# Kernel optimization log

Measured on AMD Instinct MI355X. Metric: run time of the kernel, lower is better.

Reference implementation:

```python
import jax, jax.numpy as jnp
import numpy as np

B, T, D, H = 4, 2048, 1024, 16
HD = D // H  # 64


def setup_inputs() -> dict:
    key = jax.random.key(0)
    ks = jax.random.split(key, 5)
    return {
        "x": jax.random.normal(ks[0], (B, T, D), dtype=jnp.float32),
        "W_qkv": jax.random.normal(ks[1], (D, 3 * D), dtype=jnp.float32) * 0.02,
        "b_qkv": jax.random.normal(ks[2], (3 * D,), dtype=jnp.float32) * 0.02,
        "W_out": jax.random.normal(ks[3], (D, D), dtype=jnp.float32) * 0.02,
        "b_out": jax.random.normal(ks[4], (D,), dtype=jnp.float32) * 0.02,
        "mask": 1,
    }


def reference(x, W_qkv, b_qkv, W_out, b_out, mask):
    # fused QKV projection: (B,T,3D)
    qkv = x @ W_qkv + b_qkv
    # torch layout: view (B,T,H,3*hd) then chunk last dim into q,k,v
    qkv = qkv.reshape(B, T, H, 3, HD)
    q = qkv[..., 0, :].transpose(0, 2, 1, 3)  # (B,H,T,hd)
    k = qkv[..., 1, :].transpose(0, 2, 1, 3)
    v = qkv[..., 2, :].transpose(0, 2, 1, 3)
    scores = jnp.einsum('bhqd,bhkd->bhqk', q, k) / jnp.sqrt(jnp.float32(HD))
    if mask:
        causal = jnp.triu(jnp.ones((T, T), dtype=bool), k=1)
        scores = jnp.where(causal[None, None], jnp.float32(-jnp.inf), scores)
    attn = jax.nn.softmax(scores, axis=-1)
    out = jnp.einsum('bhqk,bhkd->bhqd', attn, v)  # (B,H,T,hd)
    out = out.transpose(0, 2, 1, 3).reshape(B, T, D)
    return out @ W_out + b_out
```

## Files before the change

kernel.cpp:

```cpp
#include <hip/hip_runtime.h>

typedef unsigned short u16;
typedef __bf16 bf16x8 __attribute__((ext_vector_type(8)));
typedef float f32x4 __attribute__((ext_vector_type(4)));
typedef float f32x16 __attribute__((ext_vector_type(16)));

#define DEV __device__ __forceinline__

constexpr int Bb = 4, Tt = 2048, Dd = 1024, Hh = 16, HDd = 64;
constexpr int MM = Bb * Tt;
constexpr float QSCALE = 0.125f * 1.4426950408889634f;

DEV u16 f2bf(float f) {
  unsigned u = __float_as_uint(f);
  u += 0x7fffu + ((u >> 16) & 1u);
  return (u16)(u >> 16);
}

DEV unsigned cvtpk(float a, float b) {
  unsigned r;
  asm("v_cvt_pk_bf16_f32 %0, %1, %2" : "=v"(r) : "v"(a), "v"(b));
  return r;
}

DEV void pswap(unsigned& a, unsigned& b) {
  asm("v_permlane32_swap_b32 %0, %1" : "+v"(a), "+v"(b));
}

DEV void gload_lds16(const u16* g, u16* l) {
  __builtin_amdgcn_global_load_lds(
      (const __attribute__((address_space(1))) void*)g,
      (__attribute__((address_space(3))) void*)l, 16, 0, 0);
}

__global__ __launch_bounds__(256) void cast_x_kernel(const float* __restrict__ in,
                                                     u16* __restrict__ out, int n8) {
  int i = blockIdx.x * 256 + threadIdx.x;
  if (i >= n8) return;
  const float4* p = (const float4*)in + (size_t)i * 2;
  float4 v0 = p[0], v1 = p[1];
  union { u16 u[8]; uint4 v; } t;
  t.u[0] = f2bf(v0.x); t.u[1] = f2bf(v0.y); t.u[2] = f2bf(v0.z); t.u[3] = f2bf(v0.w);
  t.u[4] = f2bf(v1.x); t.u[5] = f2bf(v1.y); t.u[6] = f2bf(v1.z); t.u[7] = f2bf(v1.w);
  ((uint4*)out)[i] = t.v;
}

__global__ __launch_bounds__(256) void wcast_t_kernel(const float* __restrict__ in,
                                                      u16* __restrict__ out, int K, int N) {
  __shared__ float tile[32][33];
  int n0 = blockIdx.x * 32, k0 = blockIdx.y * 32;
  int tx = threadIdx.x & 31, ty = threadIdx.x >> 5;
  #pragma unroll
  for (int yy = ty; yy < 32; yy += 8)
    tile[yy][tx] = in[(size_t)(k0 + yy) * N + n0 + tx];
  __syncthreads();
  #pragma unroll
  for (int yy = ty; yy < 32; yy += 8)
    out[(size_t)(n0 + yy) * K + k0 + tx] = f2bf(tile[tx][yy]);
}

__global__ __launch_bounds__(256) void vtrans_kernel(const u16* __restrict__ V,
                                                     u16* __restrict__ Vt) {
  __shared__ u16 tile[32][33];
  size_t base = (size_t)blockIdx.z * Tt * HDd;
  int t0 = blockIdx.x * 32, d0 = blockIdx.y * 32;
  int tx = threadIdx.x & 31, ty = threadIdx.x >> 5;
  #pragma unroll
  for (int yy = ty; yy < 32; yy += 8)
    tile[yy][tx] = V[base + (size_t)(t0 + yy) * HDd + d0 + tx];
  __syncthreads();
  #pragma unroll
  for (int yy = ty; yy < 32; yy += 8)
    Vt[base + (size_t)(d0 + yy) * Tt + t0 + tx] = tile[tx][yy];
}

DEV void stage_tile(const u16* __restrict__ src, int row0, int k0, int ld, u16* lds) {
  int t = threadIdx.x, w = t >> 6;
  #pragma unroll
  for (int j = 0; j < 2; ++j) {
    int e = (j * 256 + t) * 8;
    int r = e >> 5;
    int slot = (e >> 3) & 3;
    int c = (slot ^ ((r >> 1) & 3)) << 3;
    gload_lds16(src + (size_t)(row0 + r) * ld + k0 + c, lds + j * 2048 + w * 512);
  }
}

template <int EPI>
__global__ __launch_bounds__(256) void gemm_bt_kernel(
    const u16* __restrict__ A, const u16* __restrict__ Bt,
    const float* __restrict__ bias, float* __restrict__ Cf,
    u16* __restrict__ Qb, u16* __restrict__ Kb, u16* __restrict__ Vb,
    int M, int N, int Kd) {
  __shared__ __align__(16) u16 As[2][4096];
  __shared__ __align__(16) u16 Bs[2][4096];
  int m0 = blockIdx.y * 128, n0 = blockIdx.x * 128;
  int tid = threadIdx.x, l = tid & 63, w = tid >> 6;
  int lo = l & 15, g = l >> 4;
  int wm = (w >> 1) * 64, wn = (w & 1) * 64;
  f32x4 acc[4][4] = {};
  stage_tile(A, m0, 0, Kd, As[0]);
  stage_tile(Bt, n0, 0, Kd, Bs[0]);
  __syncthreads();
  int nk = Kd >> 5;
  for (int kt = 0; kt < nk; ++kt) {
    int cur = kt & 1;
    if (kt + 1 < nk) {
      stage_tile(A, m0, (kt + 1) * 32, Kd, As[cur ^ 1]);
      stage_tile(Bt, n0, (kt + 1) * 32, Kd, Bs[cur ^ 1]);
    }
    bf16x8 a[4], b[4];
    #pragma unroll
    for (int i = 0; i < 4; ++i) {
      int row = wm + i * 16 + lo;
      a[i] = *(const bf16x8*)&As[cur][row * 32 + ((g ^ ((row >> 1) & 3)) << 3)];
    }
    #pragma unroll
    for (int j = 0; j < 4; ++j) {
      int row = wn + j * 16 + lo;
      b[j] = *(const bf16x8*)&Bs[cur][row * 32 + ((g ^ ((row >> 1) & 3)) << 3)];
    }
    #pragma unroll
    for (int i = 0; i < 4; ++i)
      #pragma unroll
      for (int j = 0; j < 4; ++j)
        acc[i][j] = __builtin_amdgcn_mfma_f32_16x16x32_bf16(a[i], b[j], acc[i][j], 0, 0, 0);
    __syncthreads();
  }
  #pragma unroll
  for (int j = 0; j < 4; ++j) {
    int n = n0 + wn + j * 16 + lo;
    float bv = bias[n];
    #pragma unroll
    for (int i = 0; i < 4; ++i) {
      #pragma unroll
      for (int r = 0; r < 4; ++r) {
        int m = m0 + wm + i * 16 + g * 4 + r;
        float v = acc[i][j][r] + bv;
        if (EPI == 0) {
          int b_ = m >> 11, t = m & (Tt - 1);
          int h = n / 192, sub = n - h * 192;
          int which = sub >> 6, d = sub & 63;
          size_t idx = ((size_t)(b_ * Hh + h) * Tt + t) * HDd + d;
          if (which == 0)      Qb[idx] = f2bf(v * QSCALE);
          else if (which == 1) Kb[idx] = f2bf(v);
          else                 Vb[idx] = f2bf(v);
        } else {
          Cf[(size_t)m * N + n] = v;
        }
      }
    }
  }
}

DEV void stage64x64(const u16* __restrict__ g, size_t rstride, u16* lds) {
  int t = threadIdx.x, w = t >> 6;
  #pragma unroll
  for (int j = 0; j < 2; ++j) {
    int e = j * 256 + t;
    int r = e >> 3, p = e & 7;
    int lg = p ^ (r & 7);
    gload_lds16(g + (size_t)r * rstride + lg * 8, lds + (size_t)(j * 256 + w * 64) * 8);
  }
}

DEV void build_pfrags(const f32x16& s, bf16x8& f0, bf16x8& f1) {
  unsigned w0 = cvtpk(s[0], s[1]),  w1 = cvtpk(s[2], s[3]);
  unsigned w2 = cvtpk(s[4], s[5]),  w3 = cvtpk(s[6], s[7]);
  unsigned w4 = cvtpk(s[8], s[9]),  w5 = cvtpk(s[10], s[11]);
  unsigned w6 = cvtpk(s[12], s[13]), w7 = cvtpk(s[14], s[15]);
  pswap(w0, w2);
  pswap(w1, w3);
  pswap(w4, w6);
  pswap(w5, w7);
  union { unsigned u[4]; bf16x8 v; } t0, t1;
  t0.u[0] = w0; t0.u[1] = w1; t0.u[2] = w2; t0.u[3] = w3;
  t1.u[0] = w4; t1.u[1] = w5; t1.u[2] = w6; t1.u[3] = w7;
  f0 = t0.v; f1 = t1.v;
}

DEV void write_o(u16* __restrict__ O, size_t rowbase, const f32x16& o0,
                 const f32x16& o1, float L, int hf) {
  float inv = 1.0f / L;
  #pragma unroll
  for (int m = 0; m < 4; ++m) {
    uint2 v0, v1;
    v0.x = cvtpk(o0[4 * m] * inv,     o0[4 * m + 1] * inv);
    v0.y = cvtpk(o0[4 * m + 2] * inv, o0[4 * m + 3] * inv);
    *(uint2*)(O + rowbase + m * 8 + hf * 4) = v0;
    v1.x = cvtpk(o1[4 * m] * inv,     o1[4 * m + 1] * inv);
    v1.y = cvtpk(o1[4 * m + 2] * inv, o1[4 * m + 3] * inv);
    *(uint2*)(O + rowbase + 32 + m * 8 + hf * 4) = v1;
  }
}

__global__ __launch_bounds__(256) void attn_kernel(const u16* __restrict__ Q,
                                                   const u16* __restrict__ K,
                                                   const u16* __restrict__ Vt,
                                                   u16* __restrict__ O) {
  __shared__ __align__(16) u16 Ks[2][4096];
  __shared__ __align__(16) u16 Vs[2][4096];
  int bh = blockIdx.y;
  int b_ = bh >> 4, h = bh & 15;
  const u16* Qp = Q + (size_t)bh * Tt * HDd;
  const u16* Kp = K + (size_t)bh * Tt * HDd;
  const u16* Vp = Vt + (size_t)bh * HDd * Tt;
  int tid = threadIdx.x, w = tid >> 6, l = tid & 63;
  int lq = l & 31, hf = l >> 5;
  int p = blockIdx.x;
  int JA = 15 - p, JB = p;
  int ntA = 2 * JA + 2, ntB = 2 * JB + 2, ntT = ntA + ntB;

  int q0 = 128 * JA + 32 * w;
  int qrow = q0 + lq;

  bf16x8 aq[4];
  #pragma unroll
  for (int s = 0; s < 4; ++s)
    aq[s] = *(const bf16x8*)(Qp + (size_t)qrow * HDd + s * 16 + hf * 8);

  f32x16 o0 = {}, o1 = {};
  float M = -1e30f, L = 0.f;

  stage64x64(Kp, HDd, Ks[0]);
  stage64x64(Vp, Tt, Vs[0]);
  __syncthreads();

  for (int it = 0; it < ntT; ++it) {
    if (it == ntA) {
      size_t rbA = ((size_t)b_ * Tt + qrow) * Dd + h * HDd;
      write_o(O, rbA, o0, o1, L, hf);
      #pragma unroll
      for (int r = 0; r < 16; ++r) { o0[r] = 0.f; o1[r] = 0.f; }
      M = -1e30f; L = 0.f;
      q0 = 128 * JB + 32 * w;
      qrow = q0 + lq;
      #pragma unroll
      for (int s = 0; s < 4; ++s)
        aq[s] = *(const bf16x8*)(Qp + (size_t)qrow * HDd + s * 16 + hf * 8);
    }
    int kt = (it < ntA ? it : it - ntA) * 64;
    int cur = it & 1;
    if (it + 1 < ntT) {
      int nkt = (it + 1 < ntA ? it + 1 : it + 1 - ntA) * 64;
      stage64x64(Kp + (size_t)nkt * HDd, HDd, Ks[cur ^ 1]);
      stage64x64(Vp + nkt, Tt, Vs[cur ^ 1]);
    }
    if (kt < q0 + 32) {
      f32x16 s0 = {}, s1 = {};
      int swz = lq & 7;
      __builtin_amdgcn_s_setprio(1);
      #pragma unroll
      for (int ds = 0; ds < 4; ++ds) {
        int slot = 2 * ds + hf;
        bf16x8 k0 = *(const bf16x8*)&Ks[cur][lq * 64 + ((slot ^ swz) << 3)];
        bf16x8 k1 = *(const bf16x8*)&Ks[cur][(32 + lq) * 64 + ((slot ^ swz) << 3)];
        s0 = __builtin_amdgcn_mfma_f32_32x32x16_bf16(k0, aq[ds], s0, 0, 0, 0);
        s1 = __builtin_amdgcn_mfma_f32_32x32x16_bf16(k1, aq[ds], s1, 0, 0, 0);
      }
      __builtin_amdgcn_s_setprio(0);
      if (kt + 63 > q0) {
        #pragma unroll
        for (int r = 0; r < 16; ++r) {
          int kg = kt + (r & 3) + 8 * (r >> 2) + 4 * hf;
          if (kg > qrow)      s0[r] = -INFINITY;
          if (kg + 32 > qrow) s1[r] = -INFINITY;
        }
      }
      float mx_[16];
      #pragma unroll
      for (int r = 0; r < 16; ++r) mx_[r] = fmaxf(s0[r], s1[r]);
      #pragma unroll
      for (int st = 8; st >= 1; st >>= 1)
        #pragma unroll
        for (int r = 0; r < 16; ++r) if (r < st) mx_[r] = fmaxf(mx_[r], mx_[r + st]);
      float mx = fmaxf(mx_[0], __shfl_xor(mx_[0], 32));
      float Mn = fmaxf(M, mx);
      float sc = __builtin_amdgcn_exp2f(M - Mn);
      M = Mn;
      #pragma unroll
      for (int r = 0; r < 16; ++r) {
        s0[r] = __builtin_amdgcn_exp2f(s0[r] - Mn);
        s1[r] = __builtin_amdgcn_exp2f(s1[r] - Mn);
      }
      float ls_[16];
      #pragma unroll
      for (int r = 0; r < 16; ++r) ls_[r] = s0[r] + s1[r];
      #pragma unroll
      for (int st = 8; st >= 1; st >>= 1)
        #pragma unroll
        for (int r = 0; r < 16; ++r) if (r < st) ls_[r] += ls_[r + st];
      float ls = ls_[0] + __shfl_xor(ls_[0], 32);
      L = L * sc + ls;
      bf16x8 pf0, pf1, pf2, pf3;
      build_pfrags(s0, pf0, pf1);
      build_pfrags(s1, pf2, pf3);
      #pragma unroll
      for (int r = 0; r < 16; ++r) { o0[r] *= sc; o1[r] *= sc; }
      __builtin_amdgcn_s_setprio(1);
      #pragma unroll
      for (int ks = 0; ks < 4; ++ks) {
        int slot = 2 * ks + hf;
        bf16x8 v0 = *(const bf16x8*)&Vs[cur][lq * 64 + ((slot ^ swz) << 3)];
        bf16x8 v1 = *(const bf16x8*)&Vs[cur][(32 + lq) * 64 + ((slot ^ swz) << 3)];
        bf16x8 pf = (ks == 0) ? pf0 : (ks == 1) ? pf1 : (ks == 2) ? pf2 : pf3;
        o0 = __builtin_amdgcn_mfma_f32_32x32x16_bf16(v0, pf, o0, 0, 0, 0);
        o1 = __builtin_amdgcn_mfma_f32_32x32x16_bf16(v1, pf, o1, 0, 0, 0);
      }
      __builtin_amdgcn_s_setprio(0);
    }
    __syncthreads();
  }

  size_t rbB = ((size_t)b_ * Tt + qrow) * Dd + h * HDd;
  write_o(O, rbB, o0, o1, L, hf);
}

extern "C" void kernel_launch(void* const* d_in, const int* in_sizes, int n_in,
                              void* d_out, int out_size, void* d_ws, size_t ws_size,
                              hipStream_t stream) {
  const float* x    = (const float*)d_in[0];
  const float* Wqkv = (const float*)d_in[1];
  const float* bqkv = (const float*)d_in[2];
  const float* Wout = (const float*)d_in[3];
  const float* bout = (const float*)d_in[4];
  float* out = (float*)d_out;
  char* ws = (char*)d_ws;

  u16* xb    = (u16*)(ws + 0);
  u16* Wqkvt = (u16*)(ws + 16777216);
  u16* Woutt = (u16*)(ws + 23068672);
  u16* Qb    = (u16*)(ws + 25165824);
  u16* Kb    = (u16*)(ws + 41943040);
  u16* Vb    = (u16*)(ws + 58720256);
  u16* Vtb   = (u16*)(ws + 0);
  u16* Ob    = (u16*)(ws + 58720256);

  cast_x_kernel<<<4096, 256, 0, stream>>>(x, xb, (MM * Dd) / 8);
  wcast_t_kernel<<<dim3(96, 32), 256, 0, stream>>>(Wqkv, Wqkvt, Dd, 3 * Dd);
  wcast_t_kernel<<<dim3(32, 32), 256, 0, stream>>>(Wout, Woutt, Dd, Dd);
  gemm_bt_kernel<0><<<dim3(24, 64), 256, 0, stream>>>(
      xb, Wqkvt, bqkv, nullptr, Qb, Kb, Vb, MM, 3 * Dd, Dd);
  vtrans_kernel<<<dim3(Tt / 32, HDd / 32, Bb * Hh), 256, 0, stream>>>(Vb, Vtb);
  attn_kernel<<<dim3(8, Bb * Hh), 256, 0, stream>>>(Qb, Kb, Vtb, Ob);
  gemm_bt_kernel<1><<<dim3(8, 64), 256, 0, stream>>>(
      Ob, Woutt, bout, out, nullptr, nullptr, nullptr, MM, Dd, Dd);
}
```

Measured before the change: 205.1 us.

## Stage QKV epilogue through LDS, swizzle GEMM tile order, skip lazy softmax rescale

The QKV GEMM epilogue now writes bf16 results into a swizzled LDS buffer per wave, then stores coalesced 16-byte rows to the head-major Q/K/V layout. Previously each lane did scattered 2-byte stores. Workgroup IDs are remapped so that neighbouring blocks share A/B tiles for better L2 reuse. The flash-attention loop skips the running-max update and output rescale unless the new max exceeds the old one by more than 8 (log2 units), trading a small overflow-headroom risk for fewer rescales.

```diff
diff --git a/kernel.cpp b/kernel.cpp
--- a/kernel.cpp
+++ b/kernel.cpp
@@ -92,33 +92,39 @@
     const float* __restrict__ bias, float* __restrict__ Cf,
     u16* __restrict__ Qb, u16* __restrict__ Kb, u16* __restrict__ Vb,
     int M, int N, int Kd) {
-  __shared__ __align__(16) u16 As[2][4096];
-  __shared__ __align__(16) u16 Bs[2][4096];
-  int m0 = blockIdx.y * 128, n0 = blockIdx.x * 128;
+  __shared__ __align__(16) u16 SH[16384];
+  int nx = N >> 7;
+  int bid = blockIdx.y * nx + blockIdx.x;
+  int nwg = (M >> 7) * nx;
+  int swz = (bid & 7) * (nwg >> 3) + (bid >> 3);
+  int m0 = (swz / nx) * 128, n0 = (swz % nx) * 128;
+
   int tid = threadIdx.x, l = tid & 63, w = tid >> 6;
   int lo = l & 15, g = l >> 4;
   int wm = (w >> 1) * 64, wn = (w & 1) * 64;
   f32x4 acc[4][4] = {};
-  stage_tile(A, m0, 0, Kd, As[0]);
-  stage_tile(Bt, n0, 0, Kd, Bs[0]);
+  stage_tile(A, m0, 0, Kd, SH);
+  stage_tile(Bt, n0, 0, Kd, SH + 8192);
   __syncthreads();
   int nk = Kd >> 5;
   for (int kt = 0; kt < nk; ++kt) {
     int cur = kt & 1;
     if (kt + 1 < nk) {
-      stage_tile(A, m0, (kt + 1) * 32, Kd, As[cur ^ 1]);
-      stage_tile(Bt, n0, (kt + 1) * 32, Kd, Bs[cur ^ 1]);
-    }
+      stage_tile(A, m0, (kt + 1) * 32, Kd, SH + (cur ^ 1) * 4096);
+      stage_tile(Bt, n0, (kt + 1) * 32, Kd, SH + 8192 + (cur ^ 1) * 4096);
+    }
+    const u16* Ac = SH + cur * 4096;
+    const u16* Bc = SH + 8192 + cur * 4096;
     bf16x8 a[4], b[4];
     #pragma unroll
     for (int i = 0; i < 4; ++i) {
       int row = wm + i * 16 + lo;
-      a[i] = *(const bf16x8*)&As[cur][row * 32 + ((g ^ ((row >> 1) & 3)) << 3)];
+      a[i] = *(const bf16x8*)&Ac[row * 32 + ((g ^ ((row >> 1) & 3)) << 3)];
     }
     #pragma unroll
     for (int j = 0; j < 4; ++j) {
       int row = wn + j * 16 + lo;
-      b[j] = *(const bf16x8*)&Bs[cur][row * 32 + ((g ^ ((row >> 1) & 3)) << 3)];
+      b[j] = *(const bf16x8*)&Bc[row * 32 + ((g ^ ((row >> 1) & 3)) << 3)];
     }
     #pragma unroll
     for (int i = 0; i < 4; ++i)
@@ -127,26 +133,48 @@
         acc[i][j] = __builtin_amdgcn_mfma_f32_16x16x32_bf16(a[i], b[j], acc[i][j], 0, 0, 0);
     __syncthreads();
   }
-  #pragma unroll
-  for (int j = 0; j < 4; ++j) {
-    int n = n0 + wn + j * 16 + lo;
-    float bv = bias[n];
-    #pragma unroll
-    for (int i = 0; i < 4; ++i) {
-      #pragma unroll
-      for (int r = 0; r < 4; ++r) {
-        int m = m0 + wm + i * 16 + g * 4 + r;
-        float v = acc[i][j][r] + bv;
-        if (EPI == 0) {
-          int b_ = m >> 11, t = m & (Tt - 1);
-          int h = n / 192, sub = n - h * 192;
-          int which = sub >> 6, d = sub & 63;
-          size_t idx = ((size_t)(b_ * Hh + h) * Tt + t) * HDd + d;
-          if (which == 0)      Qb[idx] = f2bf(v * QSCALE);
-          else if (which == 1) Kb[idx] = f2bf(v);
-          else                 Vb[idx] = f2bf(v);
-        } else {
-          Cf[(size_t)m * N + n] = v;
+  if (EPI == 0) {
+    u16* ep = SH + w * 4096;
+    int nblk = n0 + wn;
+    int hh = nblk / 192, which = (nblk % 192) >> 6;
+    float qs = (which == 0) ? QSCALE : 1.0f;
+    #pragma unroll
+    for (int j = 0; j < 4; ++j) {
+      float bv = bias[nblk + j * 16 + lo];
+      int slot = j * 2 + (lo >> 3);
+      #pragma unroll
+      for (int i = 0; i < 4; ++i) {
+        #pragma unroll
+        for (int r = 0; r < 4; ++r) {
+          int lrow = i * 16 + g * 4 + r;
+          ep[lrow * 64 + ((slot ^ (lrow & 7)) << 3) + (lo & 7)] =
+              f2bf((acc[i][j][r] + bv) * qs);
+        }
+      }
+    }
+    asm volatile("s_waitcnt lgkmcnt(0)" ::: "memory");
+    u16* dst = (which == 0) ? Qb : (which == 1) ? Kb : Vb;
+    int mblk = m0 + wm;
+    int b_ = mblk >> 11, t0 = mblk & (Tt - 1);
+    dst += ((size_t)(b_ * Hh + hh) * Tt + t0) * HDd;
+    #pragma unroll
+    for (int s = 0; s < 8; ++s) {
+      int row = s * 8 + (l >> 3);
+      int phys = ((l & 7) ^ (row & 7)) << 3;
+      uint4 v = *(const uint4*)&ep[row * 64 + phys];
+      *(uint4*)(dst + row * 64 + (l & 7) * 8) = v;
+    }
+  } else {
+    #pragma unroll
+    for (int j = 0; j < 4; ++j) {
+      int n = n0 + wn + j * 16 + lo;
+      float bv = bias[n];
+      #pragma unroll
+      for (int i = 0; i < 4; ++i) {
+        #pragma unroll
+        for (int r = 0; r < 4; ++r) {
+          int m = m0 + wm + i * 16 + g * 4 + r;
+          Cf[(size_t)m * N + n] = acc[i][j][r] + bv;
         }
       }
     }
@@ -275,13 +303,18 @@
         #pragma unroll
         for (int r = 0; r < 16; ++r) if (r < st) mx_[r] = fmaxf(mx_[r], mx_[r + st]);
       float mx = fmaxf(mx_[0], __shfl_xor(mx_[0], 32));
-      float Mn = fmaxf(M, mx);
-      float sc = __builtin_amdgcn_exp2f(M - Mn);
-      M = Mn;
+      float sc = 1.f;
+      if (!__all(mx <= M + 8.f)) {
+        float Mn = fmaxf(M, mx);
+        sc = __builtin_amdgcn_exp2f(M - Mn);
+        M = Mn;
+        #pragma unroll
+        for (int r = 0; r < 16; ++r) { o0[r] *= sc; o1[r] *= sc; }
+      }
       #pragma unroll
       for (int r = 0; r < 16; ++r) {
-        s0[r] = __builtin_amdgcn_exp2f(s0[r] - Mn);
-        s1[r] = __builtin_amdgcn_exp2f(s1[r] - Mn);
+        s0[r] = __builtin_amdgcn_exp2f(s0[r] - M);
+        s1[r] = __builtin_amdgcn_exp2f(s1[r] - M);
       }
       float ls_[16];
       #pragma unroll
@@ -295,8 +328,6 @@
       bf16x8 pf0, pf1, pf2, pf3;
       build_pfrags(s0, pf0, pf1);
       build_pfrags(s1, pf2, pf3);
-      #pragma unroll
-      for (int r = 0; r < 16; ++r) { o0[r] *= sc; o1[r] *= sc; }
       __builtin_amdgcn_s_setprio(1);
       #pragma unroll
       for (int ks = 0; ks < 4; ++ks) {
```

After: 188.7 us. -8.0%, faster.
